# Kernel optimization log

Hardware: AMD Instinct MI355X
Metric: run time of the kernel (lower is better)

The kernel has to match this reference:

```python
import jax, jax.numpy as jnp
import numpy as np

FORCE = 8.0
N_STATE = 40
BATCH = 524288


def setup_inputs() -> dict:
    key = jax.random.key(0)
    x0 = jax.random.normal(key, (BATCH, N_STATE), dtype=jnp.float32)
    t = jnp.float32(0.0)          # unused: system is autonomous (torch code passes nan)
    dt = jnp.float32(0.05)        # canonical Lorenz96 RK4 step
    return {"x0": x0, "t": t, "dt": dt}


def _dxdt(x):
    # torch shift(x, n) == roll(x, -n, dims=-1)
    # dxdt = (shift(x,1) - shift(x,-2)) * shift(x,-1) - x + force
    return (jnp.roll(x, -1, axis=-1) - jnp.roll(x, 2, axis=-1)) * jnp.roll(x, 1, axis=-1) - x + FORCE


def reference(x0, t, dt):
    # Classic RK4 step (rk4_torch); t is ignored (autonomous RHS).
    k1 = _dxdt(x0)
    k2 = _dxdt(x0 + 0.5 * dt * k1)
    k3 = _dxdt(x0 + 0.5 * dt * k2)
    k4 = _dxdt(x0 + dt * k3)
    return x0 + (dt / 6.0) * (k1 + 2.0 * k2 + 2.0 * k3 + k4)
```

## Files before the change

kernel.cpp:

```cpp
#include <hip/hip_runtime.h>


#define FORCE 8.0f

__global__ __launch_bounds__(256)
void lorenz96_rk4_shfl(const float4* __restrict__ x0,
                       const float* __restrict__ dt_p,
                       float4* __restrict__ out,
                       long nf4)
{
    const long tid  = (long)blockIdx.x * blockDim.x + threadIdx.x;
    const long wave = tid >> 6;
    const int  lane = (int)(tid & 63);
    const int  lrow = lane / 10;
    const int  c    = lane - lrow * 10;
    const long f    = wave * 60 + lane;
    const bool active = (lane < 60) && (f < nf4);

    const int lL = lrow * 10 + (c == 0 ? 9 : c - 1);
    const int lR = lrow * 10 + (c == 9 ? 0 : c + 1);

    const float dt  = dt_p[0];
    const float hdt = 0.5f * dt;

    float4 v = make_float4(0.f, 0.f, 0.f, 0.f);
    if (active) v = x0[f];
    const float x0r = v.x, x1r = v.y, x2r = v.z, x3r = v.w;

    auto deriv = [&](float s0, float s1, float s2, float s3,
                     float& d0, float& d1, float& d2, float& d3) {
        float hL2 = __shfl(s2, lL);
        float hL3 = __shfl(s3, lL);
        float hR0 = __shfl(s0, lR);
        d0 = (s1  - hL2) * hL3 - s0 + FORCE;
        d1 = (s2  - hL3) * s0  - s1 + FORCE;
        d2 = (s3  - s0 ) * s1  - s2 + FORCE;
        d3 = (hR0 - s1 ) * s2  - s3 + FORCE;
    };

    float k0, k1, k2, k3;
    float a0, a1, a2, a3;
    float y0, y1, y2, y3;

    deriv(x0r, x1r, x2r, x3r, k0, k1, k2, k3);
    a0 = k0; a1 = k1; a2 = k2; a3 = k3;
    y0 = x0r + hdt * k0; y1 = x1r + hdt * k1;
    y2 = x2r + hdt * k2; y3 = x3r + hdt * k3;

    deriv(y0, y1, y2, y3, k0, k1, k2, k3);
    a0 += 2.0f * k0; a1 += 2.0f * k1; a2 += 2.0f * k2; a3 += 2.0f * k3;
    y0 = x0r + hdt * k0; y1 = x1r + hdt * k1;
    y2 = x2r + hdt * k2; y3 = x3r + hdt * k3;

    deriv(y0, y1, y2, y3, k0, k1, k2, k3);
    a0 += 2.0f * k0; a1 += 2.0f * k1; a2 += 2.0f * k2; a3 += 2.0f * k3;
    y0 = x0r + dt * k0; y1 = x1r + dt * k1;
    y2 = x2r + dt * k2; y3 = x3r + dt * k3;

    deriv(y0, y1, y2, y3, k0, k1, k2, k3);
    a0 += k0; a1 += k1; a2 += k2; a3 += k3;

    const float s = dt * (1.0f / 6.0f);
    float4 r;
    r.x = x0r + s * a0;
    r.y = x1r + s * a1;
    r.z = x2r + s * a2;
    r.w = x3r + s * a3;
    if (active) out[f] = r;
}

extern "C" void kernel_launch(void* const* d_in, const int* in_sizes, int n_in,
                              void* d_out, int out_size, void* d_ws, size_t ws_size,
                              hipStream_t stream) {
    const float4* x0 = (const float4*)d_in[0];
    const float* dt = (const float*)d_in[2];
    float4* out = (float4*)d_out;

    const long nf4 = (long)in_sizes[0] / 4;
    const long nwaves = (nf4 + 59) / 60;
    const int block = 256;
    const long grid = (nwaves + 3) / 4;
    lorenz96_rk4_shfl<<<dim3((unsigned)grid), dim3(block), 0, stream>>>(x0, dt, out, nf4);
}
```

Baseline: 147.3 us.

## Replace wave shuffles with shared-memory halo exchange in 320-thread blocks

Each 10-thread row previously lived inside a wave, and only 60 of 64 lanes did useful work. The kernel now uses 320-thread blocks, so every thread is active, and exchanges neighbour values through double-buffered shared arrays with block barriers instead of cross-lane shuffles. This removes the idle lanes (about 6% of the wave) and keeps loads and stores fully contiguous. In exchange it adds LDS traffic and four __syncthreads per thread, which may limit overlap in this memory-bound kernel.

```diff
diff --git a/kernel.cpp b/kernel.cpp
--- a/kernel.cpp
+++ b/kernel.cpp
@@ -3,70 +3,86 @@
 
 #define FORCE 8.0f
 
-__global__ __launch_bounds__(256)
-void lorenz96_rk4_shfl(const float4* __restrict__ x0,
-                       const float* __restrict__ dt_p,
-                       float4* __restrict__ out,
-                       long nf4)
+__global__ __launch_bounds__(320)
+void lorenz96_rk4_blk(const float4* __restrict__ x0,
+                      const float* __restrict__ dt_p,
+                      float4* __restrict__ out,
+                      long nf4)
 {
-    const long tid  = (long)blockIdx.x * blockDim.x + threadIdx.x;
-    const long wave = tid >> 6;
-    const int  lane = (int)(tid & 63);
-    const int  lrow = lane / 10;
-    const int  c    = lane - lrow * 10;
-    const long f    = wave * 60 + lane;
-    const bool active = (lane < 60) && (f < nf4);
+    const int  t = threadIdx.x;
+    const long g = (long)blockIdx.x * 320 + t;
+    const bool act = (g < nf4);
 
-    const int lL = lrow * 10 + (c == 0 ? 9 : c - 1);
-    const int lR = lrow * 10 + (c == 9 ? 0 : c + 1);
+    const int e  = t % 10;
+    const int tl = (e == 0) ? t + 9 : t - 1;
+    const int tr = (e == 9) ? t - 9 : t + 1;
+
+    __shared__ float pA0[320], pA2[320], pA3[320];
+    __shared__ float pB0[320], pB2[320], pB3[320];
 
     const float dt  = dt_p[0];
     const float hdt = 0.5f * dt;
+    const float s6  = dt * (1.0f / 6.0f);
 
     float4 v = make_float4(0.f, 0.f, 0.f, 0.f);
-    if (active) v = x0[f];
+    if (act) v = x0[g];
     const float x0r = v.x, x1r = v.y, x2r = v.z, x3r = v.w;
 
-    auto deriv = [&](float s0, float s1, float s2, float s3,
-                     float& d0, float& d1, float& d2, float& d3) {
-        float hL2 = __shfl(s2, lL);
-        float hL3 = __shfl(s3, lL);
-        float hR0 = __shfl(s0, lR);
-        d0 = (s1  - hL2) * hL3 - s0 + FORCE;
-        d1 = (s2  - hL3) * s0  - s1 + FORCE;
-        d2 = (s3  - s0 ) * s1  - s2 + FORCE;
-        d3 = (hR0 - s1 ) * s2  - s3 + FORCE;
-    };
+    float y0, y1, y2, y3;
+    float a0, a1, a2, a3;
+    float k0, k1, k2, k3;
+    float hL2, hL3, hR0;
 
-    float k0, k1, k2, k3;
-    float a0, a1, a2, a3;
-    float y0, y1, y2, y3;
-
-    deriv(x0r, x1r, x2r, x3r, k0, k1, k2, k3);
+    pA0[t] = x0r; pA2[t] = x2r; pA3[t] = x3r;
+    __syncthreads();
+    hL2 = pA2[tl]; hL3 = pA3[tl]; hR0 = pA0[tr];
+    k0 = (x1r - hL2) * hL3 - x0r + FORCE;
+    k1 = (x2r - hL3) * x0r - x1r + FORCE;
+    k2 = (x3r - x0r) * x1r - x2r + FORCE;
+    k3 = (hR0 - x1r) * x2r - x3r + FORCE;
     a0 = k0; a1 = k1; a2 = k2; a3 = k3;
     y0 = x0r + hdt * k0; y1 = x1r + hdt * k1;
     y2 = x2r + hdt * k2; y3 = x3r + hdt * k3;
 
-    deriv(y0, y1, y2, y3, k0, k1, k2, k3);
+    pB0[t] = y0; pB2[t] = y2; pB3[t] = y3;
+    __syncthreads();
+    hL2 = pB2[tl]; hL3 = pB3[tl]; hR0 = pB0[tr];
+    k0 = (y1 - hL2) * hL3 - y0 + FORCE;
+    k1 = (y2 - hL3) * y0 - y1 + FORCE;
+    k2 = (y3 - y0) * y1 - y2 + FORCE;
+    k3 = (hR0 - y1) * y2 - y3 + FORCE;
     a0 += 2.0f * k0; a1 += 2.0f * k1; a2 += 2.0f * k2; a3 += 2.0f * k3;
     y0 = x0r + hdt * k0; y1 = x1r + hdt * k1;
     y2 = x2r + hdt * k2; y3 = x3r + hdt * k3;
 
-    deriv(y0, y1, y2, y3, k0, k1, k2, k3);
+    pA0[t] = y0; pA2[t] = y2; pA3[t] = y3;
+    __syncthreads();
+    hL2 = pA2[tl]; hL3 = pA3[tl]; hR0 = pA0[tr];
+    k0 = (y1 - hL2) * hL3 - y0 + FORCE;
+    k1 = (y2 - hL3) * y0 - y1 + FORCE;
+    k2 = (y3 - y0) * y1 - y2 + FORCE;
+    k3 = (hR0 - y1) * y2 - y3 + FORCE;
     a0 += 2.0f * k0; a1 += 2.0f * k1; a2 += 2.0f * k2; a3 += 2.0f * k3;
     y0 = x0r + dt * k0; y1 = x1r + dt * k1;
     y2 = x2r + dt * k2; y3 = x3r + dt * k3;
 
-    deriv(y0, y1, y2, y3, k0, k1, k2, k3);
+    pB0[t] = y0; pB2[t] = y2; pB3[t] = y3;
+    __syncthreads();
+    hL2 = pB2[tl]; hL3 = pB3[tl]; hR0 = pB0[tr];
+    k0 = (y1 - hL2) * hL3 - y0 + FORCE;
+    k1 = (y2 - hL3) * y0 - y1 + FORCE;
+    k2 = (y3 - y0) * y1 - y2 + FORCE;
+    k3 = (hR0 - y1) * y2 - y3 + FORCE;
     a0 += k0; a1 += k1; a2 += k2; a3 += k3;
 
-    const float s = dt * (1.0f / 6.0f);
-    float4 r;
-    r.x = x0r + s * a0;
-    r.y = x1r + s * a1;
-    r.z = x2r + s * a2;
-    r.w = x3r + s * a3;
-    if (active) out[f] = r;
+    if (act) {
+        float4 r;
+        r.x = x0r + s6 * a0;
+        r.y = x1r + s6 * a1;
+        r.z = x2r + s6 * a2;
+        r.w = x3r + s6 * a3;
+        out[g] = r;
+    }
 }
 
 extern "C" void kernel_launch(void* const* d_in, const int* in_sizes, int n_in,
@@ -77,8 +93,6 @@
     float4* out = (float4*)d_out;
 
     const long nf4 = (long)in_sizes[0] / 4;
-    const long nwaves = (nf4 + 59) / 60;
-    const int block = 256;
-    const long grid = (nwaves + 3) / 4;
-    lorenz96_rk4_shfl<<<dim3((unsigned)grid), dim3(block), 0, stream>>>(x0, dt, out, nf4);
+    const long grid = (nf4 + 319) / 320;
+    lorenz96_rk4_blk<<<dim3((unsigned)grid), dim3(320), 0, stream>>>(x0, dt, out, nf4);
 }
```

New measurement: 148.8 us. Within noise of the previous version (+1.0%).
